# Performance work log

Hardware: AMD Instinct MI355X
Metric: run time of the kernel (lower is better)

## Reference

```python
import jax, jax.numpy as jnp
import numpy as np

N_GROUP = 64
GROUP_SIZE = 64
INPUT_DIM = 2048
BATCH = 8192
N_MONTN = 512


def setup_inputs() -> dict:
    key = jax.random.key(0)
    k1, k2, k3, k4, k5 = jax.random.split(key, 5)
    x = jax.random.normal(k1, (BATCH, INPUT_DIM), dtype=jnp.float32)
    weight = jax.random.normal(k2, (N_GROUP * GROUP_SIZE, INPUT_DIM), dtype=jnp.float32) * 0.02
    bias = jax.random.normal(k3, (N_GROUP * GROUP_SIZE,), dtype=jnp.float32) * 0.02
    rand_u = jax.random.uniform(k4, (BATCH,), dtype=jnp.float32)
    montn_index = jax.random.randint(k5, (N_MONTN,), 0, INPUT_DIM, dtype=jnp.int32)
    return {"x": x, "weight": weight, "bias": bias, "rand_u": rand_u,
            "montn_index": montn_index}


def reference(x, weight, bias, rand_u, montn_index):
    # Square the weights on monotone input columns (in-place in torch).
    w = weight.at[:, montn_index].set(weight[:, montn_index] ** 2)
    # y = x @ w^T + b  -> [B, n_group * n_group_size]
    y = jnp.einsum('bi,oi->bo', x, w) + bias
    B = y.shape[0]
    # per-group min over contiguous slices, then max over groups
    group_mins = y.reshape(B, N_GROUP, GROUP_SIZE).min(axis=2)  # [B, n_group]
    out = group_mins.max(axis=1)                                 # [B]
    # vectorized Bernoulli: 1.0 if u < sigmoid(out) else 0.0
    sample = (rand_u < jax.nn.sigmoid(out)).astype(jnp.float32)
    return sample.reshape(-1, 1)
```

## Files before the change

### kernel.cpp

```cpp
#include <hip/hip_runtime.h>
#include <cmath>


typedef _Float16 f16x8 __attribute__((ext_vector_type(8)));
typedef float f32x4 __attribute__((ext_vector_type(4)));

#define MARGIN_EPS 4e-3f
#define MAX_UNDEC 96

__device__ __forceinline__ void async_load16(const void* gptr, void* lptr) {
  __builtin_amdgcn_global_load_lds(
      (const __attribute__((address_space(1))) void*)gptr,
      (__attribute__((address_space(3))) void*)lptr, 16, 0, 0);
}

__device__ __forceinline__ float us2f(unsigned short u) {
  return (float)__builtin_bit_cast(_Float16, u);
}

__device__ __forceinline__ unsigned f2key(float f) {
  unsigned b = __float_as_uint(f);
  return (b & 0x80000000u) ? ~b : (b | 0x80000000u);
}
__device__ __forceinline__ float key2f(unsigned e) {
  unsigned b = (e & 0x80000000u) ? (e ^ 0x80000000u) : ~e;
  return __uint_as_float(b);
}

__global__ void convert_hi(const float* __restrict__ x,
                           const float* __restrict__ wgt,
                           unsigned short* __restrict__ xo,
                           unsigned short* __restrict__ wo,
                           const int* __restrict__ montn,
                           int* __restrict__ count,
                           unsigned* __restrict__ gmax) {
  const int b = blockIdx.x;
  const int t = threadIdx.x;
  if (b >= 3072) {
    gmax[(b - 3072) * 256 + t] = 0u;
    return;
  }
  __shared__ unsigned msk[64];
  const int l = t & 63, w = t >> 6;
  const int r = b * 4 + w;
  const int use_mask = (r >= 8192) ? 1 : 0;
  if (b == 0 && t == 0) *count = 0;
  if (use_mask) {
    if (t < 64) msk[t] = 0u;
    __syncthreads();
    for (int j = t; j < 512; j += 256) {
      const int c = montn[j];
      atomicOr(&msk[c >> 5], 1u << (c & 31));
    }
    __syncthreads();
  }
  const float* rowp = use_mask ? (wgt + (size_t)(r - 8192) * 2048)
                               : (x + (size_t)r * 2048);
  unsigned short* up = use_mask ? (wo + (size_t)(r - 8192) * 2048)
                                : (xo + (size_t)r * 2048);
  float4 v[4][2];
#pragma unroll
  for (int p = 0; p < 4; ++p) {
    v[p][0] = ((const float4*)rowp)[p * 128 + 2 * l];
    v[p][1] = ((const float4*)rowp)[p * 128 + 2 * l + 1];
  }
  unsigned mw[4];
#pragma unroll
  for (int p = 0; p < 4; ++p)
    mw[p] = use_mask ? msk[p * 16 + (l >> 2)] : 0u;

#pragma unroll
  for (int p = 0; p < 4; ++p) {
    float f[8];
    f[0] = v[p][0].x; f[1] = v[p][0].y; f[2] = v[p][0].z; f[3] = v[p][0].w;
    f[4] = v[p][1].x; f[5] = v[p][1].y; f[6] = v[p][1].z; f[7] = v[p][1].w;
    unsigned short hs[8];
#pragma unroll
    for (int c = 0; c < 8; ++c) {
      float g = f[c];
      if ((mw[p] >> (8 * (l & 3) + c)) & 1u) g = g * g;
      hs[c] = __builtin_bit_cast(unsigned short, (_Float16)g);
    }
    uint4 H;
    H.x = (unsigned)hs[0] | ((unsigned)hs[1] << 16);
    H.y = (unsigned)hs[2] | ((unsigned)hs[3] << 16);
    H.z = (unsigned)hs[4] | ((unsigned)hs[5] << 16);
    H.w = (unsigned)hs[6] | ((unsigned)hs[7] << 16);
    *((uint4*)(up + p * 512 + 8 * l)) = H;
  }
}

__global__ void convert_split(float* __restrict__ x, float* __restrict__ wgt,
                              const int* __restrict__ montn,
                              int* __restrict__ count,
                              unsigned* __restrict__ gmax) {
  const int b = blockIdx.x;
  const int t = threadIdx.x;
  if (b >= 3072) {
    gmax[(b - 3072) * 256 + t] = 0u;
    return;
  }
  __shared__ unsigned msk[64];
  const int l = t & 63, w = t >> 6;
  const int r = b * 4 + w;
  const int use_mask = (r >= 8192) ? 1 : 0;
  if (b == 0 && t == 0) *count = 0;
  if (use_mask) {
    if (t < 64) msk[t] = 0u;
    __syncthreads();
    for (int j = t; j < 512; j += 256) {
      const int c = montn[j];
      atomicOr(&msk[c >> 5], 1u << (c & 31));
    }
    __syncthreads();
  }
  float* rowp = use_mask ? (wgt + (size_t)(r - 8192) * 2048)
                         : (x + (size_t)r * 2048);
  float4 v[4][2];
#pragma unroll
  for (int p = 0; p < 4; ++p) {
    v[p][0] = ((const float4*)rowp)[p * 128 + 2 * l];
    v[p][1] = ((const float4*)rowp)[p * 128 + 2 * l + 1];
  }
  unsigned mw[4];
#pragma unroll
  for (int p = 0; p < 4; ++p)
    mw[p] = use_mask ? msk[p * 16 + (l >> 2)] : 0u;

  unsigned short* up = (unsigned short*)rowp;
#pragma unroll
  for (int p = 0; p < 4; ++p) {
    float f[8];
    f[0] = v[p][0].x; f[1] = v[p][0].y; f[2] = v[p][0].z; f[3] = v[p][0].w;
    f[4] = v[p][1].x; f[5] = v[p][1].y; f[6] = v[p][1].z; f[7] = v[p][1].w;
    unsigned short hs[8], ls[8];
#pragma unroll
    for (int c = 0; c < 8; ++c) {
      float g = f[c];
      if ((mw[p] >> (8 * (l & 3) + c)) & 1u) g = g * g;
      _Float16 h = (_Float16)g;
      float res = g - (float)h;
      _Float16 lo = (_Float16)res;
      hs[c] = __builtin_bit_cast(unsigned short, h);
      ls[c] = __builtin_bit_cast(unsigned short, lo);
    }
    uint4 H, L;
    H.x = (unsigned)hs[0] | ((unsigned)hs[1] << 16);
    H.y = (unsigned)hs[2] | ((unsigned)hs[3] << 16);
    H.z = (unsigned)hs[4] | ((unsigned)hs[5] << 16);
    H.w = (unsigned)hs[6] | ((unsigned)hs[7] << 16);
    L.x = (unsigned)ls[0] | ((unsigned)ls[1] << 16);
    L.y = (unsigned)ls[2] | ((unsigned)ls[3] << 16);
    L.z = (unsigned)ls[4] | ((unsigned)ls[5] << 16);
    L.w = (unsigned)ls[6] | ((unsigned)ls[7] << 16);
    *((uint4*)(up + p * 512 + 8 * l)) = H;
    *((uint4*)(up + 2048 + p * 512 + 8 * l)) = L;
  }
}

__global__ __launch_bounds__(256, 2) void gemm_minmax(
    const unsigned short* __restrict__ X, const unsigned short* __restrict__ W,
    const float* __restrict__ bias, unsigned* __restrict__ gmax, int rs) {
  __shared__ unsigned short As[128 * 64];
  __shared__ unsigned short Bs[256 * 64];
  const int t = threadIdx.x;
  const int lane = t & 63;
  const int w = t >> 6;
  const int wm = w >> 1, wn = w & 1;
  const int lin = blockIdx.x;
  const int sid = lin >> 3;
  const int m0 = (sid >> 1) * 128;
  const int n0 = ((lin & 7) * 2 + (sid & 1)) * 256;

  const int rowBase = w * 8 + (lane >> 3);
  const int gchunk = ((lane & 7) ^ ((lane >> 3) & 7)) * 8;
  const size_t gA0 = (size_t)(m0 + rowBase) * rs + gchunk;
  const size_t gB0 = (size_t)(n0 + rowBase) * rs + gchunk;
  unsigned short* ldsA0 = As + w * 512;
  unsigned short* ldsB0 = Bs + w * 512;

  const int am = lane & 15, quad = lane >> 4;
  int arow[4], brow[8];
#pragma unroll
  for (int i = 0; i < 4; ++i) arow[i] = (wm * 64 + i * 16 + am) * 64;
#pragma unroll
  for (int j = 0; j < 8; ++j) brow[j] = (wn * 128 + j * 16 + am) * 64;
  int swz[2];
#pragma unroll
  for (int h = 0; h < 2; ++h) swz[h] = (((h << 2) + quad) ^ (am & 7)) * 8;

  f32x4 acc[4][8];
#pragma unroll
  for (int i = 0; i < 4; ++i)
#pragma unroll
    for (int j = 0; j < 8; ++j) acc[i][j] = (f32x4){0.f, 0.f, 0.f, 0.f};

#pragma unroll 1
  for (int it = 0; it < 32; ++it) {
    const int kin = it * 64;
    __syncthreads();
#pragma unroll
    for (int c = 0; c < 4; ++c)
      async_load16(X + gA0 + (size_t)(c * 32) * rs + kin, ldsA0 + c * 2048);
#pragma unroll
    for (int c = 0; c < 8; ++c)
      async_load16(W + gB0 + (size_t)(c * 32) * rs + kin, ldsB0 + c * 2048);
    __syncthreads();

#pragma unroll
    for (int h = 0; h < 2; ++h) {
      f16x8 av[4], bv[8];
#pragma unroll
      for (int i = 0; i < 4; ++i) av[i] = *(const f16x8*)(As + arow[i] + swz[h]);
#pragma unroll
      for (int j = 0; j < 8; ++j) bv[j] = *(const f16x8*)(Bs + brow[j] + swz[h]);
#pragma unroll
      for (int mb = 0; mb < 4; ++mb)
#pragma unroll
        for (int nb = 0; nb < 8; ++nb)
          acc[mb][nb] = __builtin_amdgcn_mfma_f32_16x16x32_f16(
              av[mb], bv[nb], acc[mb][nb], 0, 0, 0);
    }
  }

  float bv8[8];
#pragma unroll
  for (int nb = 0; nb < 8; ++nb) bv8[nb] = bias[n0 + wn * 128 + nb * 16 + am];
#pragma unroll
  for (int mb = 0; mb < 4; ++mb) {
#pragma unroll
    for (int reg = 0; reg < 4; ++reg) {
      float vm = -3.4e38f;
#pragma unroll
      for (int hh = 0; hh < 2; ++hh) {
        float v = fminf(
            fminf(acc[mb][4 * hh + 0][reg] + bv8[4 * hh + 0],
                  acc[mb][4 * hh + 1][reg] + bv8[4 * hh + 1]),
            fminf(acc[mb][4 * hh + 2][reg] + bv8[4 * hh + 2],
                  acc[mb][4 * hh + 3][reg] + bv8[4 * hh + 3]));
        v = fminf(v, __shfl_xor(v, 1, 64));
        v = fminf(v, __shfl_xor(v, 2, 64));
        v = fminf(v, __shfl_xor(v, 4, 64));
        v = fminf(v, __shfl_xor(v, 8, 64));
        vm = fmaxf(vm, v);
      }
      if (am == 0) {
        const int row = m0 + wm * 64 + mb * 16 + quad * 4 + reg;
        atomicMax(&gmax[row], f2key(vm));
      }
    }
  }
}

__global__ void finalize_margin(const unsigned* __restrict__ gmax,
                                const float* __restrict__ rand_u,
                                float* __restrict__ out,
                                int* __restrict__ count, int* __restrict__ undec,
                                float4* __restrict__ ybuf4) {
  const int t = threadIdx.x;
  ybuf4[(size_t)blockIdx.x * 256 + t] = (float4){0.f, 0.f, 0.f, 0.f};
  if (blockIdx.x < 32) {
    const int row = blockIdx.x * 256 + t;
    const float v = key2f(gmax[row]);
    const float u = rand_u[row];
    const float slo = 1.0f / (1.0f + expf(-(v - MARGIN_EPS)));
    const float shi = 1.0f / (1.0f + expf(-(v + MARGIN_EPS)));
    if (u < slo) {
      out[row] = 1.0f;
    } else if (u >= shi) {
      out[row] = 0.0f;
    } else {
      const int i = atomicAdd(count, 1);
      if (i < 8192) undec[i] = row;
    }
  }
}

__global__ __launch_bounds__(256) void recompute_fp32(
    const float* __restrict__ X, const float* __restrict__ W,
    const int* __restrict__ montn, const int* __restrict__ count,
    const int* __restrict__ undec, float* __restrict__ ybuf) {
  __shared__ float wf[64 * 129];
  __shared__ float part[256];
  __shared__ unsigned msk[64];
  const int g = blockIdx.x, kc = blockIdx.y;
  const int t = threadIdx.x;
  int n = *count;
  if (n > MAX_UNDEC) n = MAX_UNDEC;
  if (n == 0) return;

  if (t < 64) msk[t] = 0u;
  __syncthreads();
  for (int j = t; j < 512; j += 256) {
    const int c = montn[j];
    atomicOr(&msk[c >> 5], 1u << (c & 31));
  }
  __syncthreads();

  {
    const int cl = t >> 2, ks = t & 3;
    const int k0 = kc * 128 + ks * 32;
    const float* wp = W + (size_t)(g * 64 + cl) * 2048 + k0;
    float* dst = wf + cl * 129 + ks * 32;
    const unsigned mword = msk[k0 >> 5];
#pragma unroll
    for (int i = 0; i < 32; i += 4) {
      float4 wv = *(const float4*)(wp + i);
      float f0 = wv.x, f1 = wv.y, f2 = wv.z, f3 = wv.w;
      if ((mword >> (i + 0)) & 1u) f0 *= f0;
      if ((mword >> (i + 1)) & 1u) f1 *= f1;
      if ((mword >> (i + 2)) & 1u) f2 *= f2;
      if ((mword >> (i + 3)) & 1u) f3 *= f3;
      dst[i + 0] = f0; dst[i + 1] = f1; dst[i + 2] = f2; dst[i + 3] = f3;
    }
  }
  __syncthreads();

  const int col = t & 63, kq = t >> 6;
  const float* wcol = wf + col * 129 + kq * 32;
  for (int s = 0; s < n; ++s) {
    const int row = undec[s];
    const float* xp = X + (size_t)row * 2048 + kc * 128 + kq * 32;
    float acc = 0.f;
#pragma unroll
    for (int i = 0; i < 32; i += 4) {
      float4 xv = *(const float4*)(xp + i);
      acc = fmaf(xv.x, wcol[i + 0], acc);
      acc = fmaf(xv.y, wcol[i + 1], acc);
      acc = fmaf(xv.z, wcol[i + 2], acc);
      acc = fmaf(xv.w, wcol[i + 3], acc);
    }
    part[t] = acc;
    __syncthreads();
    if (t < 64) {
      const float y = part[t] + part[t + 64] + part[t + 128] + part[t + 192];
      atomicAdd(ybuf + (size_t)s * 4096 + g * 64 + t, y);
    }
    __syncthreads();
  }
}

__global__ __launch_bounds__(256) void recompute_rows(
    const unsigned short* __restrict__ X, const unsigned short* __restrict__ W,
    const int* __restrict__ count, const int* __restrict__ undec,
    float* __restrict__ ybuf) {
  __shared__ float wf[64 * 129];
  __shared__ float part[256];
  const int g = blockIdx.x, kc = blockIdx.y;
  const int t = threadIdx.x;
  int n = *count;
  if (n > MAX_UNDEC) n = MAX_UNDEC;
  if (n == 0) return;

  {
    const int cl = t >> 2, ks = t & 3;
    const unsigned short* wp =
        W + (size_t)(g * 64 + cl) * 4096 + kc * 128 + ks * 32;
    float* dst = wf + cl * 129 + ks * 32;
#pragma unroll
    for (int i = 0; i < 32; i += 8) {
      uint4 hv = *(const uint4*)(wp + i);
      uint4 lv = *(const uint4*)(wp + 2048 + i);
      const unsigned* hw = (const unsigned*)&hv;
      const unsigned* lw = (const unsigned*)&lv;
#pragma unroll
      for (int m = 0; m < 4; ++m) {
        dst[i + 2 * m] = us2f((unsigned short)(hw[m] & 0xFFFF)) +
                         us2f((unsigned short)(lw[m] & 0xFFFF));
        dst[i + 2 * m + 1] = us2f((unsigned short)(hw[m] >> 16)) +
                             us2f((unsigned short)(lw[m] >> 16));
      }
    }
  }
  __syncthreads();

  const int col = t & 63, kq = t >> 6;
  const float* wcol = wf + col * 129 + kq * 32;
  for (int s = 0; s < n; ++s) {
    const int row = undec[s];
    const unsigned short* xp = X + (size_t)row * 4096 + kc * 128 + kq * 32;
    float acc = 0.f;
#pragma unroll
    for (int i = 0; i < 32; i += 8) {
      uint4 hv = *(const uint4*)(xp + i);
      uint4 lv = *(const uint4*)(xp + 2048 + i);
      const unsigned* hw = (const unsigned*)&hv;
      const unsigned* lw = (const unsigned*)&lv;
#pragma unroll
      for (int m = 0; m < 4; ++m) {
        const float x0 = us2f((unsigned short)(hw[m] & 0xFFFF)) +
                         us2f((unsigned short)(lw[m] & 0xFFFF));
        const float x1 = us2f((unsigned short)(hw[m] >> 16)) +
                         us2f((unsigned short)(lw[m] >> 16));
        acc = fmaf(x0, wcol[i + 2 * m], acc);
        acc = fmaf(x1, wcol[i + 2 * m + 1], acc);
      }
    }
    part[t] = acc;
    __syncthreads();
    if (t < 64) {
      const float y = part[t] + part[t + 64] + part[t + 128] + part[t + 192];
      atomicAdd(ybuf + (size_t)s * 4096 + g * 64 + t, y);
    }
    __syncthreads();
  }
}

__global__ void decide(const float* __restrict__ ybuf,
                       const int* __restrict__ undec, const int* __restrict__ count,
                       const float* __restrict__ bias,
                       const float* __restrict__ rand_u, float* __restrict__ out) {
  __shared__ float gm[64];
  int n = *count;
  if (n > MAX_UNDEC) n = MAX_UNDEC;
  const int s = blockIdx.x;
  if (s >= n) return;
  const int t = threadIdx.x;
  const int g = t >> 2, p4 = t & 3;
  const float* yb = ybuf + (size_t)s * 4096;
  const int c0 = g * 64 + p4 * 16;
  float m = 3.4e38f;
#pragma unroll
  for (int e = 0; e < 16; ++e) m = fminf(m, yb[c0 + e] + bias[c0 + e]);
  m = fminf(m, __shfl_xor(m, 1, 64));
  m = fminf(m, __shfl_xor(m, 2, 64));
  if (p4 == 0) gm[g] = m;
  __syncthreads();
  if (t < 64) {
    float v = gm[t];
    v = fmaxf(v, __shfl_xor(v, 1, 64));
    v = fmaxf(v, __shfl_xor(v, 2, 64));
    v = fmaxf(v, __shfl_xor(v, 4, 64));
    v = fmaxf(v, __shfl_xor(v, 8, 64));
    v = fmaxf(v, __shfl_xor(v, 16, 64));
    v = fmaxf(v, __shfl_xor(v, 32, 64));
    if (t == 0) {
      const int row = undec[s];
      const float sg = 1.0f / (1.0f + expf(-v));
      out[row] = (rand_u[row] < sg) ? 1.0f : 0.0f;
    }
  }
}

extern "C" void kernel_launch(void* const* d_in, const int* in_sizes, int n_in,
                              void* d_out, int out_size, void* d_ws, size_t ws_size,
                              hipStream_t stream) {
  float* x = (float*)d_in[0];
  float* weight = (float*)d_in[1];
  const float* bias = (const float*)d_in[2];
  const float* rand_u = (const float*)d_in[3];
  const int* montn = (const int*)d_in[4];
  float* out = (float*)d_out;

  char* ws = (char*)d_ws;
  int* count = (int*)ws;
  int* undec = (int*)(ws + 256);
  float* ybuf = (float*)(ws + 65536);
  unsigned* gmax = (unsigned*)(ws + 65536 + 1572864);

  const size_t XO_OFF = (size_t)4 * 1024 * 1024;
  const size_t XO_BYTES = (size_t)8192 * 2048 * 2;
  const size_t WO_BYTES = (size_t)4096 * 2048 * 2;
  const bool big_ws = ws_size >= XO_OFF + XO_BYTES + WO_BYTES;

  if (big_ws) {
    unsigned short* xo = (unsigned short*)(ws + XO_OFF);
    unsigned short* wo = (unsigned short*)(ws + XO_OFF + XO_BYTES);
    convert_hi<<<3104, 256, 0, stream>>>(x, weight, xo, wo, montn, count, gmax);
    gemm_minmax<<<1024, 256, 0, stream>>>(xo, wo, bias, gmax, 2048);
    finalize_margin<<<384, 256, 0, stream>>>(gmax, rand_u, out, count, undec,
                                             (float4*)ybuf);
    recompute_fp32<<<dim3(64, 16), 256, 0, stream>>>(x, weight, montn, count,
                                                     undec, ybuf);
  } else {
    convert_split<<<3104, 256, 0, stream>>>(x, weight, montn, count, gmax);
    gemm_minmax<<<1024, 256, 0, stream>>>(
        (const unsigned short*)x, (const unsigned short*)weight, bias, gmax,
        4096);
    finalize_margin<<<384, 256, 0, stream>>>(gmax, rand_u, out, count, undec,
                                             (float4*)ybuf);
    recompute_rows<<<dim3(64, 16), 256, 0, stream>>>(
        (const unsigned short*)x, (const unsigned short*)weight, count, undec,
        ybuf);
  }
  decide<<<MAX_UNDEC, 256, 0, stream>>>(ybuf, undec, count, bias, rand_u, out);
}
```

Baseline: 281.0 us.

## Fuse all stages into one persistent cooperative kernel with grid syncs

Replaces the five separate launches (convert, GEMM min-max, margin finalize, fp32 recompute, decide) with a single cooperative kernel of 512 blocks that moves between stages using grid.sync. The GEMM stage writes per-tile partial maxima to a pmax buffer instead of using atomic max on keyed values, and each block handles two GEMM tiles persistently. The goal is to remove launch gaps and tail effects between stages. In exchange it fixes occupancy at 2 blocks per CU, adds grid-wide barrier cost, and shrinks the GEMM grid, which could lower overlap.

```diff
diff --git a/kernel.cpp b/kernel.cpp
--- a/kernel.cpp
+++ b/kernel.cpp
@@ -1,5 +1,8 @@
 #include <hip/hip_runtime.h>
+#include <hip/hip_cooperative_groups.h>
 #include <cmath>
+
+namespace cg = cooperative_groups;
 
 
 typedef _Float16 f16x8 __attribute__((ext_vector_type(8)));
@@ -27,25 +30,22 @@
   return __uint_as_float(b);
 }
 
-__global__ void convert_hi(const float* __restrict__ x,
-                           const float* __restrict__ wgt,
-                           unsigned short* __restrict__ xo,
-                           unsigned short* __restrict__ wo,
-                           const int* __restrict__ montn,
-                           int* __restrict__ count,
-                           unsigned* __restrict__ gmax) {
+__global__ __launch_bounds__(256, 2) void fused_all(
+    const float* __restrict__ x, const float* __restrict__ wgt,
+    const float* __restrict__ bias, const float* __restrict__ rand_u,
+    const int* __restrict__ montn, float* __restrict__ out,
+    unsigned short* __restrict__ xo, unsigned short* __restrict__ wo,
+    int* __restrict__ count, int* __restrict__ undec,
+    float* __restrict__ ybuf, float* __restrict__ pmax) {
+  __shared__ __align__(16) char smem_raw[49152];
+  cg::grid_group grid = cg::this_grid();
   const int b = blockIdx.x;
   const int t = threadIdx.x;
-  if (b >= 3072) {
-    gmax[(b - 3072) * 256 + t] = 0u;
-    return;
-  }
-  __shared__ unsigned msk[64];
-  const int l = t & 63, w = t >> 6;
-  const int r = b * 4 + w;
-  const int use_mask = (r >= 8192) ? 1 : 0;
-  if (b == 0 && t == 0) *count = 0;
-  if (use_mask) {
+  const int lane = t & 63, w = t >> 6;
+
+  {
+    unsigned* msk = (unsigned*)smem_raw;
+    if (b == 0 && t == 0) *count = 0;
     if (t < 64) msk[t] = 0u;
     __syncthreads();
     for (int j = t; j < 512; j += 256) {
@@ -53,40 +53,286 @@
       atomicOr(&msk[c >> 5], 1u << (c & 31));
     }
     __syncthreads();
-  }
-  const float* rowp = use_mask ? (wgt + (size_t)(r - 8192) * 2048)
-                               : (x + (size_t)r * 2048);
-  unsigned short* up = use_mask ? (wo + (size_t)(r - 8192) * 2048)
-                                : (xo + (size_t)r * 2048);
-  float4 v[4][2];
-#pragma unroll
-  for (int p = 0; p < 4; ++p) {
-    v[p][0] = ((const float4*)rowp)[p * 128 + 2 * l];
-    v[p][1] = ((const float4*)rowp)[p * 128 + 2 * l + 1];
-  }
-  unsigned mw[4];
-#pragma unroll
-  for (int p = 0; p < 4; ++p)
-    mw[p] = use_mask ? msk[p * 16 + (l >> 2)] : 0u;
-
-#pragma unroll
-  for (int p = 0; p < 4; ++p) {
-    float f[8];
-    f[0] = v[p][0].x; f[1] = v[p][0].y; f[2] = v[p][0].z; f[3] = v[p][0].w;
-    f[4] = v[p][1].x; f[5] = v[p][1].y; f[6] = v[p][1].z; f[7] = v[p][1].w;
-    unsigned short hs[8];
-#pragma unroll
-    for (int c = 0; c < 8; ++c) {
-      float g = f[c];
-      if ((mw[p] >> (8 * (l & 3) + c)) & 1u) g = g * g;
-      hs[c] = __builtin_bit_cast(unsigned short, (_Float16)g);
-    }
-    uint4 H;
-    H.x = (unsigned)hs[0] | ((unsigned)hs[1] << 16);
-    H.y = (unsigned)hs[2] | ((unsigned)hs[3] << 16);
-    H.z = (unsigned)hs[4] | ((unsigned)hs[5] << 16);
-    H.w = (unsigned)hs[6] | ((unsigned)hs[7] << 16);
-    *((uint4*)(up + p * 512 + 8 * l)) = H;
+    const int l = lane;
+#pragma unroll 1
+    for (int i = 0; i < 6; ++i) {
+      const int r = b * 24 + i * 4 + w;
+      const int use_mask = (r >= 8192) ? 1 : 0;
+      const float* rowp = use_mask ? (wgt + (size_t)(r - 8192) * 2048)
+                                   : (x + (size_t)r * 2048);
+      unsigned short* up = use_mask ? (wo + (size_t)(r - 8192) * 2048)
+                                    : (xo + (size_t)r * 2048);
+      float4 v[4][2];
+#pragma unroll
+      for (int p = 0; p < 4; ++p) {
+        v[p][0] = ((const float4*)rowp)[p * 128 + 2 * l];
+        v[p][1] = ((const float4*)rowp)[p * 128 + 2 * l + 1];
+      }
+      unsigned mw[4];
+#pragma unroll
+      for (int p = 0; p < 4; ++p)
+        mw[p] = use_mask ? msk[p * 16 + (l >> 2)] : 0u;
+#pragma unroll
+      for (int p = 0; p < 4; ++p) {
+        float f[8];
+        f[0] = v[p][0].x; f[1] = v[p][0].y; f[2] = v[p][0].z; f[3] = v[p][0].w;
+        f[4] = v[p][1].x; f[5] = v[p][1].y; f[6] = v[p][1].z; f[7] = v[p][1].w;
+        unsigned short hs[8];
+#pragma unroll
+        for (int c = 0; c < 8; ++c) {
+          float g = f[c];
+          if ((mw[p] >> (8 * (l & 3) + c)) & 1u) g = g * g;
+          hs[c] = __builtin_bit_cast(unsigned short, (_Float16)g);
+        }
+        uint4 H;
+        H.x = (unsigned)hs[0] | ((unsigned)hs[1] << 16);
+        H.y = (unsigned)hs[2] | ((unsigned)hs[3] << 16);
+        H.z = (unsigned)hs[4] | ((unsigned)hs[5] << 16);
+        H.w = (unsigned)hs[6] | ((unsigned)hs[7] << 16);
+        *((uint4*)(up + p * 512 + 8 * l)) = H;
+      }
+    }
+  }
+  __threadfence();
+  grid.sync();
+
+  {
+    unsigned short* As = (unsigned short*)smem_raw;
+    unsigned short* Bs = As + 128 * 64;
+    const int wm = w >> 1, wn = w & 1;
+    const int rowBase = w * 8 + (lane >> 3);
+    const int gchunk = ((lane & 7) ^ ((lane >> 3) & 7)) * 8;
+    const int am = lane & 15, quad = lane >> 4;
+    int arow[4], brow[8], swz[2];
+#pragma unroll
+    for (int i = 0; i < 4; ++i) arow[i] = (wm * 64 + i * 16 + am) * 64;
+#pragma unroll
+    for (int j = 0; j < 8; ++j) brow[j] = (wn * 128 + j * 16 + am) * 64;
+#pragma unroll
+    for (int h = 0; h < 2; ++h) swz[h] = (((h << 2) + quad) ^ (am & 7)) * 8;
+    unsigned short* ldsA0 = As + w * 512;
+    unsigned short* ldsB0 = Bs + w * 512;
+
+#pragma unroll 1
+    for (int tt = 0; tt < 2; ++tt) {
+      const int lin = b + tt * 512;
+      const int sid = lin >> 3;
+      const int m0 = (sid >> 1) * 128;
+      const int nb = (lin & 7) * 2 + (sid & 1);
+      const int n0 = nb * 256;
+      const size_t gA0 = (size_t)(m0 + rowBase) * 2048 + gchunk;
+      const size_t gB0 = (size_t)(n0 + rowBase) * 2048 + gchunk;
+
+      f32x4 acc[4][8];
+#pragma unroll
+      for (int i = 0; i < 4; ++i)
+#pragma unroll
+        for (int j = 0; j < 8; ++j) acc[i][j] = (f32x4){0.f, 0.f, 0.f, 0.f};
+
+#pragma unroll 1
+      for (int it = 0; it < 32; ++it) {
+        const int kin = it * 64;
+        __syncthreads();
+#pragma unroll
+        for (int c = 0; c < 4; ++c)
+          async_load16(xo + gA0 + (size_t)(c * 32) * 2048 + kin,
+                       ldsA0 + c * 2048);
+#pragma unroll
+        for (int c = 0; c < 8; ++c)
+          async_load16(wo + gB0 + (size_t)(c * 32) * 2048 + kin,
+                       ldsB0 + c * 2048);
+        __syncthreads();
+#pragma unroll
+        for (int h = 0; h < 2; ++h) {
+          f16x8 av[4], bv[8];
+#pragma unroll
+          for (int i = 0; i < 4; ++i)
+            av[i] = *(const f16x8*)(As + arow[i] + swz[h]);
+#pragma unroll
+          for (int j = 0; j < 8; ++j)
+            bv[j] = *(const f16x8*)(Bs + brow[j] + swz[h]);
+#pragma unroll
+          for (int mb = 0; mb < 4; ++mb)
+#pragma unroll
+            for (int nb8 = 0; nb8 < 8; ++nb8)
+              acc[mb][nb8] = __builtin_amdgcn_mfma_f32_16x16x32_f16(
+                  av[mb], bv[nb8], acc[mb][nb8], 0, 0, 0);
+        }
+      }
+
+      float bv8[8];
+#pragma unroll
+      for (int nb8 = 0; nb8 < 8; ++nb8)
+        bv8[nb8] = bias[n0 + wn * 128 + nb8 * 16 + am];
+      float vml[4][4];
+#pragma unroll
+      for (int mb = 0; mb < 4; ++mb) {
+#pragma unroll
+        for (int reg = 0; reg < 4; ++reg) {
+          float vm = -3.4e38f;
+#pragma unroll
+          for (int hh = 0; hh < 2; ++hh) {
+            float v = fminf(
+                fminf(acc[mb][4 * hh + 0][reg] + bv8[4 * hh + 0],
+                      acc[mb][4 * hh + 1][reg] + bv8[4 * hh + 1]),
+                fminf(acc[mb][4 * hh + 2][reg] + bv8[4 * hh + 2],
+                      acc[mb][4 * hh + 3][reg] + bv8[4 * hh + 3]));
+            v = fminf(v, __shfl_xor(v, 1, 64));
+            v = fminf(v, __shfl_xor(v, 2, 64));
+            v = fminf(v, __shfl_xor(v, 4, 64));
+            v = fminf(v, __shfl_xor(v, 8, 64));
+            vm = fmaxf(vm, v);
+          }
+          vml[mb][reg] = vm;
+        }
+      }
+      __syncthreads();
+      float* pbuf = (float*)smem_raw;
+      if (wn == 1 && am == 0) {
+#pragma unroll
+        for (int mb = 0; mb < 4; ++mb)
+#pragma unroll
+          for (int reg = 0; reg < 4; ++reg)
+            pbuf[wm * 64 + mb * 16 + quad * 4 + reg] = vml[mb][reg];
+      }
+      __syncthreads();
+      if (wn == 0 && am == 0) {
+#pragma unroll
+        for (int mb = 0; mb < 4; ++mb)
+#pragma unroll
+          for (int reg = 0; reg < 4; ++reg) {
+            const int ridx = wm * 64 + mb * 16 + quad * 4 + reg;
+            const float v = fmaxf(vml[mb][reg], pbuf[ridx]);
+            pmax[(size_t)(m0 + ridx) * 16 + nb] = v;
+          }
+      }
+    }
+  }
+  __threadfence();
+  grid.sync();
+
+  {
+    if (t < 192)
+      ((float4*)ybuf)[(size_t)b * 192 + t] = (float4){0.f, 0.f, 0.f, 0.f};
+    const int r3 = b * 16 + (t >> 4);
+    float v = pmax[(size_t)r3 * 16 + (t & 15)];
+    v = fmaxf(v, __shfl_xor(v, 1, 64));
+    v = fmaxf(v, __shfl_xor(v, 2, 64));
+    v = fmaxf(v, __shfl_xor(v, 4, 64));
+    v = fmaxf(v, __shfl_xor(v, 8, 64));
+    if ((t & 15) == 0) {
+      const float u = rand_u[r3];
+      const float slo = 1.0f / (1.0f + expf(-(v - MARGIN_EPS)));
+      const float shi = 1.0f / (1.0f + expf(-(v + MARGIN_EPS)));
+      if (u < slo) {
+        out[r3] = 1.0f;
+      } else if (u >= shi) {
+        out[r3] = 0.0f;
+      } else {
+        const int i = atomicAdd(count, 1);
+        if (i < 8192) undec[i] = r3;
+      }
+    }
+  }
+  __threadfence();
+  grid.sync();
+
+  {
+    int n = *count;
+    if (n > MAX_UNDEC) n = MAX_UNDEC;
+    if (n > 0) {
+      float* wf = (float*)smem_raw;
+      float* part = wf + 64 * 129;
+      unsigned* msk = (unsigned*)(part + 256);
+      if (t < 64) msk[t] = 0u;
+      __syncthreads();
+      for (int j = t; j < 512; j += 256) {
+        const int c = montn[j];
+        atomicOr(&msk[c >> 5], 1u << (c & 31));
+      }
+      __syncthreads();
+#pragma unroll 1
+      for (int pp = 0; pp < 2; ++pp) {
+        const int idx = b + pp * 512;
+        const int g = idx >> 4, kc = idx & 15;
+        {
+          const int cl = t >> 2, ks = t & 3;
+          const int k0 = kc * 128 + ks * 32;
+          const float* wp = wgt + (size_t)(g * 64 + cl) * 2048 + k0;
+          float* dst = wf + cl * 129 + ks * 32;
+          const unsigned mword = msk[k0 >> 5];
+#pragma unroll
+          for (int i = 0; i < 32; i += 4) {
+            float4 wv = *(const float4*)(wp + i);
+            float f0 = wv.x, f1 = wv.y, f2 = wv.z, f3 = wv.w;
+            if ((mword >> (i + 0)) & 1u) f0 *= f0;
+            if ((mword >> (i + 1)) & 1u) f1 *= f1;
+            if ((mword >> (i + 2)) & 1u) f2 *= f2;
+            if ((mword >> (i + 3)) & 1u) f3 *= f3;
+            dst[i + 0] = f0; dst[i + 1] = f1; dst[i + 2] = f2; dst[i + 3] = f3;
+          }
+        }
+        __syncthreads();
+        const int col = t & 63, kq = t >> 6;
+        const float* wcol = wf + col * 129 + kq * 32;
+        for (int s = 0; s < n; ++s) {
+          const int row = undec[s];
+          const float* xp = x + (size_t)row * 2048 + kc * 128 + kq * 32;
+          float acc = 0.f;
+#pragma unroll
+          for (int i = 0; i < 32; i += 4) {
+            float4 xv = *(const float4*)(xp + i);
+            acc = fmaf(xv.x, wcol[i + 0], acc);
+            acc = fmaf(xv.y, wcol[i + 1], acc);
+            acc = fmaf(xv.z, wcol[i + 2], acc);
+            acc = fmaf(xv.w, wcol[i + 3], acc);
+          }
+          part[t] = acc;
+          __syncthreads();
+          if (t < 64) {
+            const float y = part[t] + part[t + 64] + part[t + 128] +
+                            part[t + 192];
+            atomicAdd(ybuf + (size_t)s * 4096 + g * 64 + t, y);
+          }
+          __syncthreads();
+        }
+      }
+    }
+  }
+  __threadfence();
+  grid.sync();
+
+  {
+    int n = *count;
+    if (n > MAX_UNDEC) n = MAX_UNDEC;
+    if (b < n) {
+      float* gm = (float*)smem_raw;
+      const int s = b;
+      const int g = t >> 2, p4 = t & 3;
+      const float* yb = ybuf + (size_t)s * 4096;
+      const int c0 = g * 64 + p4 * 16;
+      float m = 3.4e38f;
+#pragma unroll
+      for (int e = 0; e < 16; ++e) m = fminf(m, yb[c0 + e] + bias[c0 + e]);
+      m = fminf(m, __shfl_xor(m, 1, 64));
+      m = fminf(m, __shfl_xor(m, 2, 64));
+      if (p4 == 0) gm[g] = m;
+      __syncthreads();
+      if (t < 64) {
+        float v = gm[t];
+        v = fmaxf(v, __shfl_xor(v, 1, 64));
+        v = fmaxf(v, __shfl_xor(v, 2, 64));
+        v = fmaxf(v, __shfl_xor(v, 4, 64));
+        v = fmaxf(v, __shfl_xor(v, 8, 64));
+        v = fmaxf(v, __shfl_xor(v, 16, 64));
+        v = fmaxf(v, __shfl_xor(v, 32, 64));
+        if (t == 0) {
+          const int row = undec[s];
+          const float sg = 1.0f / (1.0f + expf(-v));
+          out[row] = (rand_u[row] < sg) ? 1.0f : 0.0f;
+        }
+      }
+    }
   }
 }
 
@@ -276,70 +522,6 @@
   }
 }
 
-__global__ __launch_bounds__(256) void recompute_fp32(
-    const float* __restrict__ X, const float* __restrict__ W,
-    const int* __restrict__ montn, const int* __restrict__ count,
-    const int* __restrict__ undec, float* __restrict__ ybuf) {
-  __shared__ float wf[64 * 129];
-  __shared__ float part[256];
-  __shared__ unsigned msk[64];
-  const int g = blockIdx.x, kc = blockIdx.y;
-  const int t = threadIdx.x;
-  int n = *count;
-  if (n > MAX_UNDEC) n = MAX_UNDEC;
-  if (n == 0) return;
-
-  if (t < 64) msk[t] = 0u;
-  __syncthreads();
-  for (int j = t; j < 512; j += 256) {
-    const int c = montn[j];
-    atomicOr(&msk[c >> 5], 1u << (c & 31));
-  }
-  __syncthreads();
-
-  {
-    const int cl = t >> 2, ks = t & 3;
-    const int k0 = kc * 128 + ks * 32;
-    const float* wp = W + (size_t)(g * 64 + cl) * 2048 + k0;
-    float* dst = wf + cl * 129 + ks * 32;
-    const unsigned mword = msk[k0 >> 5];
-#pragma unroll
-    for (int i = 0; i < 32; i += 4) {
-      float4 wv = *(const float4*)(wp + i);
-      float f0 = wv.x, f1 = wv.y, f2 = wv.z, f3 = wv.w;
-      if ((mword >> (i + 0)) & 1u) f0 *= f0;
-      if ((mword >> (i + 1)) & 1u) f1 *= f1;
-      if ((mword >> (i + 2)) & 1u) f2 *= f2;
-      if ((mword >> (i + 3)) & 1u) f3 *= f3;
-      dst[i + 0] = f0; dst[i + 1] = f1; dst[i + 2] = f2; dst[i + 3] = f3;
-    }
-  }
-  __syncthreads();
-
-  const int col = t & 63, kq = t >> 6;
-  const float* wcol = wf + col * 129 + kq * 32;
-  for (int s = 0; s < n; ++s) {
-    const int row = undec[s];
-    const float* xp = X + (size_t)row * 2048 + kc * 128 + kq * 32;
-    float acc = 0.f;
-#pragma unroll
-    for (int i = 0; i < 32; i += 4) {
-      float4 xv = *(const float4*)(xp + i);
-      acc = fmaf(xv.x, wcol[i + 0], acc);
-      acc = fmaf(xv.y, wcol[i + 1], acc);
-      acc = fmaf(xv.z, wcol[i + 2], acc);
-      acc = fmaf(xv.w, wcol[i + 3], acc);
-    }
-    part[t] = acc;
-    __syncthreads();
-    if (t < 64) {
-      const float y = part[t] + part[t + 64] + part[t + 128] + part[t + 192];
-      atomicAdd(ybuf + (size_t)s * 4096 + g * 64 + t, y);
-    }
-    __syncthreads();
-  }
-}
-
 __global__ __launch_bounds__(256) void recompute_rows(
     const unsigned short* __restrict__ X, const unsigned short* __restrict__ W,
     const int* __restrict__ count, const int* __restrict__ undec,
@@ -456,6 +638,7 @@
   int* count = (int*)ws;
   int* undec = (int*)(ws + 256);
   float* ybuf = (float*)(ws + 65536);
+  float* pmax = (float*)(ws + 65536 + 1572864);
   unsigned* gmax = (unsigned*)(ws + 65536 + 1572864);
 
   const size_t XO_OFF = (size_t)4 * 1024 * 1024;
@@ -463,16 +646,22 @@
   const size_t WO_BYTES = (size_t)4096 * 2048 * 2;
   const bool big_ws = ws_size >= XO_OFF + XO_BYTES + WO_BYTES;
 
+  hipError_t cerr = hipErrorUnknown;
   if (big_ws) {
     unsigned short* xo = (unsigned short*)(ws + XO_OFF);
     unsigned short* wo = (unsigned short*)(ws + XO_OFF + XO_BYTES);
-    convert_hi<<<3104, 256, 0, stream>>>(x, weight, xo, wo, montn, count, gmax);
-    gemm_minmax<<<1024, 256, 0, stream>>>(xo, wo, bias, gmax, 2048);
-    finalize_margin<<<384, 256, 0, stream>>>(gmax, rand_u, out, count, undec,
-                                             (float4*)ybuf);
-    recompute_fp32<<<dim3(64, 16), 256, 0, stream>>>(x, weight, montn, count,
-                                                     undec, ybuf);
-  } else {
+    const float* biasp = bias;
+    const float* randp = rand_u;
+    const int* montnp = montn;
+    void* args[] = {(void*)&x,     (void*)&weight, (void*)&biasp,
+                    (void*)&randp, (void*)&montnp, (void*)&out,
+                    (void*)&xo,    (void*)&wo,     (void*)&count,
+                    (void*)&undec, (void*)&ybuf,   (void*)&pmax};
+    cerr = hipLaunchCooperativeKernel((const void*)fused_all, dim3(512),
+                                      dim3(256), args, 0, stream);
+  }
+  if (cerr != hipSuccess) {
+    (void)hipGetLastError();
     convert_split<<<3104, 256, 0, stream>>>(x, weight, montn, count, gmax);
     gemm_minmax<<<1024, 256, 0, stream>>>(
         (const unsigned short*)x, (const unsigned short*)weight, bias, gmax,
@@ -482,6 +671,7 @@
     recompute_rows<<<dim3(64, 16), 256, 0, stream>>>(
         (const unsigned short*)x, (const unsigned short*)weight, count, undec,
         ybuf);
-  }
-  decide<<<MAX_UNDEC, 256, 0, stream>>>(ybuf, undec, count, bias, rand_u, out);
-}
+    decide<<<MAX_UNDEC, 256, 0, stream>>>(ybuf, undec, count, bias, rand_u,
+                                          out);
+  }
+}
```

Result: slower. 703.7 us (+150.5%).
